# Optimization experiments

Measured on AMD Instinct MI355X. Metric: run time of the kernel, lower is better.

The kernel has to match this reference:

```python
import jax, jax.numpy as jnp
import numpy as np

D_MODEL = 1024
BS, K = 16, 64


def setup_inputs() -> dict:
    key = jax.random.key(0)
    k1, k2 = jax.random.split(key)
    Mp_cls = jax.random.normal(k1, (BS, K, D_MODEL), dtype=jnp.float32)
    mask_p = jnp.ones((BS, K, 4, K), dtype=bool)  # unused (no rnk_transformer)
    # nn.Linear(4*d_model, 3, bias=False) weight: [3, 4*d_model]
    W = jax.random.normal(k2, (3, 4 * D_MODEL), dtype=jnp.float32) * (4 * D_MODEL) ** -0.5
    return {"Mp_cls": Mp_cls, "mask_p": mask_p, "W": W}


def reference(Mp_cls, mask_p, W):
    # Pairwise scores: feature at [b,i,j] = cat(A[b,j], A[b,i], |A[b,j]-A[b,i]|, A[b,i]*A[b,j])
    # scores = feature @ W.T  -> [bs,K,K,3]. We split W into its 4 d_model blocks
    # so the concatenated [bs,K,K,4d] tensor is never materialized.
    d = Mp_cls.shape[-1]
    W1, W2, W3, W4 = W[:, :d], W[:, d:2 * d], W[:, 2 * d:3 * d], W[:, 3 * d:]
    t1 = jnp.einsum('bjd,cd->bjc', Mp_cls, W1)[:, None, :, :]          # from unsqueeze(1).expand
    t2 = jnp.einsum('bid,cd->bic', Mp_cls, W2)[:, :, None, :]          # from unsqueeze(2).expand
    diff = jnp.abs(Mp_cls[:, None, :, :] - Mp_cls[:, :, None, :])      # [bs,K,K,d]
    t3 = jnp.einsum('bijd,cd->bijc', diff, W3)
    t4 = jnp.einsum('bid,bjd,cd->bijc', Mp_cls, Mp_cls, W4)            # elementwise product term
    return t1 + t2 + t3 + t4  # [bs, K, K, 3]
```

## Files before the change

kernel.cpp:

```cpp
#include <hip/hip_runtime.h>

#define D_MODEL 1024
#define KK 64
#define BSZ 16

__global__ __launch_bounds__(256) void precompute_rows(
    const float* __restrict__ Mp, const float* __restrict__ W,
    float* __restrict__ P12)
{
    const int wave = (blockIdx.x * 256 + threadIdx.x) >> 6;
    const int lane = threadIdx.x & 63;
    const float* row = Mp + (size_t)wave * D_MODEL;

    float s[6] = {0.f, 0.f, 0.f, 0.f, 0.f, 0.f};
#pragma unroll
    for (int k = 0; k < 4; ++k) {
        const int d = k * 256 + lane * 4;
        const float4 m = *reinterpret_cast<const float4*>(row + d);
#pragma unroll
        for (int c = 0; c < 3; ++c) {
            const float4 w1 = *reinterpret_cast<const float4*>(W + c * 4096 + d);
            const float4 w2 = *reinterpret_cast<const float4*>(W + c * 4096 + 1024 + d);
            s[c]     += m.x * w1.x + m.y * w1.y + m.z * w1.z + m.w * w1.w;
            s[3 + c] += m.x * w2.x + m.y * w2.y + m.z * w2.z + m.w * w2.w;
        }
    }
#pragma unroll
    for (int off = 32; off; off >>= 1)
#pragma unroll
        for (int t = 0; t < 6; ++t)
            s[t] += __shfl_xor(s[t], off, 64);

    if (lane < 3) {
        P12[wave * 3 + lane]        = s[lane];
        P12[3072 + wave * 3 + lane] = s[3 + lane];
    }
}

__global__ __launch_bounds__(256) void pair_kernel(
    const float* __restrict__ Mp, const float* __restrict__ W,
    const float* __restrict__ P12, float* __restrict__ out)
{
    const int b   = blockIdx.x >> 6;
    const int i   = blockIdx.x & 63;
    const int wid = threadIdx.x >> 6;
    const int lane = threadIdx.x & 63;

    const float* batch = Mp + (size_t)b * KK * D_MODEL;
    const float* rowi  = batch + i * D_MODEL;

    float4 mi[4], w3[3][4], w4[3][4];
#pragma unroll
    for (int k = 0; k < 4; ++k) {
        const int d = k * 256 + lane * 4;
        mi[k] = *reinterpret_cast<const float4*>(rowi + d);
#pragma unroll
        for (int c = 0; c < 3; ++c) {
            w3[c][k] = *reinterpret_cast<const float4*>(W + c * 4096 + 2048 + d);
            w4[c][k] = *reinterpret_cast<const float4*>(W + c * 4096 + 3072 + d);
        }
    }

    const float p2c0 = P12[3072 + (b * 64 + i) * 3 + 0];
    const float p2c1 = P12[3072 + (b * 64 + i) * 3 + 1];
    const float p2c2 = P12[3072 + (b * 64 + i) * 3 + 2];

#pragma unroll 1
    for (int jj = 0; jj < 16; ++jj) {
        const int j = wid * 16 + jj;
        const float* rowj = batch + j * D_MODEL;

        float s3[3] = {0.f, 0.f, 0.f};
        float s4[3] = {0.f, 0.f, 0.f};
#pragma unroll
        for (int k = 0; k < 4; ++k) {
            const float4 mj = *reinterpret_cast<const float4*>(rowj + k * 256 + lane * 4);
#define TERM(E)                                                                \
            {                                                                  \
                const float dabs = fabsf(mi[k].E - mj.E);                      \
                const float prod = mi[k].E * mj.E;                             \
                s3[0] += dabs * w3[0][k].E;                                    \
                s3[1] += dabs * w3[1][k].E;                                    \
                s3[2] += dabs * w3[2][k].E;                                    \
                s4[0] += prod * w4[0][k].E;                                    \
                s4[1] += prod * w4[1][k].E;                                    \
                s4[2] += prod * w4[2][k].E;                                    \
            }
            TERM(x) TERM(y) TERM(z) TERM(w)
#undef TERM
        }

#pragma unroll
        for (int off = 32; off; off >>= 1) {
#pragma unroll
            for (int t = 0; t < 3; ++t) {
                s3[t] += __shfl_xor(s3[t], off, 64);
                s4[t] += __shfl_xor(s4[t], off, 64);
            }
        }

        if (lane < 3) {
            const int c = lane;
            out[(((size_t)b * 64 + i) * 64 + j) * 3 + c] =
                P12[(b * 64 + j) * 3 + c] + ((c == 0) ? p2c0 : (c == 1) ? p2c1 : p2c2)
                + s3[c] + s4[c];
        }
    }
}

extern "C" void kernel_launch(void* const* d_in, const int* in_sizes, int n_in,
                              void* d_out, int out_size, void* d_ws, size_t ws_size,
                              hipStream_t stream)
{
    const float* Mp = (const float*)d_in[0];
    const float* W  = (const float*)d_in[2];
    float* out = (float*)d_out;
    float* P12 = (float*)d_ws;

    precompute_rows<<<256, 256, 0, stream>>>(Mp, W, P12);
    pair_kernel<<<BSZ * KK, 256, 0, stream>>>(Mp, W, P12, out);
}
```

Before: 101.3 us.

## Exploit pair symmetry to compute only upper-triangular i,j pairs

```diff
diff --git a/kernel.cpp b/kernel.cpp
--- a/kernel.cpp
+++ b/kernel.cpp
@@ -8,22 +8,19 @@
     const float* __restrict__ Mp, const float* __restrict__ W,
     float* __restrict__ P12)
 {
-    const int wave = (blockIdx.x * 256 + threadIdx.x) >> 6;
+    const int row  = blockIdx.x;
+    const int wid  = threadIdx.x >> 6;
     const int lane = threadIdx.x & 63;
-    const float* row = Mp + (size_t)wave * D_MODEL;
+    const int d    = wid * 256 + lane * 4;
 
-    float s[6] = {0.f, 0.f, 0.f, 0.f, 0.f, 0.f};
+    const float4 m = *reinterpret_cast<const float4*>(Mp + (size_t)row * D_MODEL + d);
+    float s[6];
 #pragma unroll
-    for (int k = 0; k < 4; ++k) {
-        const int d = k * 256 + lane * 4;
-        const float4 m = *reinterpret_cast<const float4*>(row + d);
-#pragma unroll
-        for (int c = 0; c < 3; ++c) {
-            const float4 w1 = *reinterpret_cast<const float4*>(W + c * 4096 + d);
-            const float4 w2 = *reinterpret_cast<const float4*>(W + c * 4096 + 1024 + d);
-            s[c]     += m.x * w1.x + m.y * w1.y + m.z * w1.z + m.w * w1.w;
-            s[3 + c] += m.x * w2.x + m.y * w2.y + m.z * w2.z + m.w * w2.w;
-        }
+    for (int c = 0; c < 3; ++c) {
+        const float4 w1 = *reinterpret_cast<const float4*>(W + c * 4096 + d);
+        const float4 w2 = *reinterpret_cast<const float4*>(W + c * 4096 + 1024 + d);
+        s[c]     = m.x * w1.x + m.y * w1.y + m.z * w1.z + m.w * w1.w;
+        s[3 + c] = m.x * w2.x + m.y * w2.y + m.z * w2.z + m.w * w2.w;
     }
 #pragma unroll
     for (int off = 32; off; off >>= 1)
@@ -31,60 +28,80 @@
         for (int t = 0; t < 6; ++t)
             s[t] += __shfl_xor(s[t], off, 64);
 
-    if (lane < 3) {
-        P12[wave * 3 + lane]        = s[lane];
-        P12[3072 + wave * 3 + lane] = s[3 + lane];
+    __shared__ float part[4][6];
+    if (lane == 0) {
+#pragma unroll
+        for (int t = 0; t < 6; ++t) part[wid][t] = s[t];
+    }
+    __syncthreads();
+    if (threadIdx.x < 6) {
+        const int t = threadIdx.x;
+        const float v = part[0][t] + part[1][t] + part[2][t] + part[3][t];
+        if (t < 3) P12[row * 3 + t]              = v;
+        else       P12[3072 + row * 3 + (t - 3)] = v;
     }
 }
 
-__global__ __launch_bounds__(256) void pair_kernel(
+__device__ __forceinline__ int tri_start(int i) { return (i * (129 - i)) >> 1; }
+
+__global__ __launch_bounds__(256, 2) void pair_kernel(
     const float* __restrict__ Mp, const float* __restrict__ W,
     const float* __restrict__ P12, float* __restrict__ out)
 {
-    const int b   = blockIdx.x >> 6;
-    const int i   = blockIdx.x & 63;
-    const int wid = threadIdx.x >> 6;
+    const int b    = blockIdx.x;
+    const int slot = blockIdx.y;
+    const int wid  = threadIdx.x >> 6;
     const int lane = threadIdx.x & 63;
 
     const float* batch = Mp + (size_t)b * KK * D_MODEL;
-    const float* rowi  = batch + i * D_MODEL;
+    float*       outb  = out + (size_t)b * KK * KK * 3;
+    const float* P1    = P12 + b * KK * 3;
+    const float* P2    = P12 + 3072 + b * KK * 3;
 
-    float4 mi[4], w3[3][4], w4[3][4];
+    float4 w3[3][4], w4[3][4];
 #pragma unroll
     for (int k = 0; k < 4; ++k) {
         const int d = k * 256 + lane * 4;
-        mi[k] = *reinterpret_cast<const float4*>(rowi + d);
 #pragma unroll
         for (int c = 0; c < 3; ++c) {
             w3[c][k] = *reinterpret_cast<const float4*>(W + c * 4096 + 2048 + d);
             w4[c][k] = *reinterpret_cast<const float4*>(W + c * 4096 + 3072 + d);
         }
     }
+#define KEEP4(f) asm volatile("" : "+v"(f.x), "+v"(f.y), "+v"(f.z), "+v"(f.w))
+#pragma unroll
+    for (int c = 0; c < 3; ++c)
+#pragma unroll
+        for (int k = 0; k < 4; ++k) { KEEP4(w3[c][k]); KEEP4(w4[c][k]); }
+#undef KEEP4
 
-    const float p2c0 = P12[3072 + (b * 64 + i) * 3 + 0];
-    const float p2c1 = P12[3072 + (b * 64 + i) * 3 + 1];
-    const float p2c2 = P12[3072 + (b * 64 + i) * 3 + 2];
+    const int p0 = slot * 32 + wid * 8;
+    int i = (int)((129.0f - sqrtf(16641.0f - 8.0f * (float)p0)) * 0.5f);
+    if (i > 63) i = 63;
+    if (i < 0)  i = 0;
+    while (tri_start(i + 1) <= p0) ++i;
+    while (tri_start(i) > p0) --i;
+    int j = i + (p0 - tri_start(i));
 
-#pragma unroll 1
-    for (int jj = 0; jj < 16; ++jj) {
-        const int j = wid * 16 + jj;
+    float4 mi[4];
+#pragma unroll
+    for (int k = 0; k < 4; ++k)
+        mi[k] = *reinterpret_cast<const float4*>(batch + i * D_MODEL + k * 256 + lane * 4);
+
+#pragma unroll 2
+    for (int t = 0; t < 8; ++t) {
         const float* rowj = batch + j * D_MODEL;
-
-        float s3[3] = {0.f, 0.f, 0.f};
-        float s4[3] = {0.f, 0.f, 0.f};
+        float sc0 = 0.f, sc1 = 0.f, sc2 = 0.f;
 #pragma unroll
         for (int k = 0; k < 4; ++k) {
             const float4 mj = *reinterpret_cast<const float4*>(rowj + k * 256 + lane * 4);
-#define TERM(E)                                                                \
-            {                                                                  \
-                const float dabs = fabsf(mi[k].E - mj.E);                      \
-                const float prod = mi[k].E * mj.E;                             \
-                s3[0] += dabs * w3[0][k].E;                                    \
-                s3[1] += dabs * w3[1][k].E;                                    \
-                s3[2] += dabs * w3[2][k].E;                                    \
-                s4[0] += prod * w4[0][k].E;                                    \
-                s4[1] += prod * w4[1][k].E;                                    \
-                s4[2] += prod * w4[2][k].E;                                    \
+#define TERM(E)                                                      \
+            {                                                        \
+                const float dabs = fabsf(mi[k].E - mj.E);            \
+                const float prod = mi[k].E * mj.E;                   \
+                sc0 += dabs * w3[0][k].E;  sc0 += prod * w4[0][k].E; \
+                sc1 += dabs * w3[1][k].E;  sc1 += prod * w4[1][k].E; \
+                sc2 += dabs * w3[2][k].E;  sc2 += prod * w4[2][k].E; \
             }
             TERM(x) TERM(y) TERM(z) TERM(w)
 #undef TERM
@@ -92,18 +109,27 @@
 
 #pragma unroll
         for (int off = 32; off; off >>= 1) {
-#pragma unroll
-            for (int t = 0; t < 3; ++t) {
-                s3[t] += __shfl_xor(s3[t], off, 64);
-                s4[t] += __shfl_xor(s4[t], off, 64);
-            }
+            sc0 += __shfl_xor(sc0, off, 64);
+            sc1 += __shfl_xor(sc1, off, 64);
+            sc2 += __shfl_xor(sc2, off, 64);
         }
 
         if (lane < 3) {
             const int c = lane;
-            out[(((size_t)b * 64 + i) * 64 + j) * 3 + c] =
-                P12[(b * 64 + j) * 3 + c] + ((c == 0) ? p2c0 : (c == 1) ? p2c1 : p2c2)
-                + s3[c] + s4[c];
+            const float sc = (c == 0) ? sc0 : (c == 1) ? sc1 : sc2;
+            outb[(i * KK + j) * 3 + c] = P1[j * 3 + c] + P2[i * 3 + c] + sc;
+            outb[(j * KK + i) * 3 + c] = P1[i * 3 + c] + P2[j * 3 + c] + sc;
+        }
+
+        ++j;
+        if (j == KK) {
+            ++i;
+            if (i < KK) {
+                j = i;
+#pragma unroll
+                for (int k = 0; k < 4; ++k)
+                    mi[k] = *reinterpret_cast<const float4*>(batch + i * D_MODEL + k * 256 + lane * 4);
+            }
         }
     }
 }
@@ -117,6 +143,6 @@
     float* out = (float*)d_out;
     float* P12 = (float*)d_ws;
 
-    precompute_rows<<<256, 256, 0, stream>>>(Mp, W, P12);
-    pair_kernel<<<BSZ * KK, 256, 0, stream>>>(Mp, W, P12, out);
+    precompute_rows<<<1024, 256, 0, stream>>>(Mp, W, P12);
+    pair_kernel<<<dim3(BSZ, 65), 256, 0, stream>>>(Mp, W, P12, out);
 }
```

Result: faster. 81.62 us (-19.4%).

## Transpose Mp per batch and map j to lanes to drop per-pair shuffle reductions

Applied to the files above, without the earlier changes.

```diff
diff --git a/kernel.cpp b/kernel.cpp
--- a/kernel.cpp
+++ b/kernel.cpp
@@ -4,106 +4,133 @@
 #define KK 64
 #define BSZ 16
 
-__global__ __launch_bounds__(256) void precompute_rows(
+__global__ __launch_bounds__(256) void prep_kernel(
     const float* __restrict__ Mp, const float* __restrict__ W,
-    float* __restrict__ P12)
+    float* __restrict__ MpT, float* __restrict__ P12)
 {
-    const int wave = (blockIdx.x * 256 + threadIdx.x) >> 6;
-    const int lane = threadIdx.x & 63;
-    const float* row = Mp + (size_t)wave * D_MODEL;
+    const int b = blockIdx.x;
+    const int y = blockIdx.y;
+    const int t = threadIdx.x;
 
-    float s[6] = {0.f, 0.f, 0.f, 0.f, 0.f, 0.f};
+    if (y < 16) {
+        __shared__ float tile[64 * 65];
+        const int d0 = y * 64;
+        const float* __restrict__ src = Mp + (size_t)b * (KK * D_MODEL);
 #pragma unroll
-    for (int k = 0; k < 4; ++k) {
-        const int d = k * 256 + lane * 4;
-        const float4 m = *reinterpret_cast<const float4*>(row + d);
+        for (int p = 0; p < 4; ++p) {
+            const int idx = p * 256 + t;
+            const int j   = idx >> 4;
+            const int c4  = (idx & 15) * 4;
+            const float4 v = *reinterpret_cast<const float4*>(src + j * D_MODEL + d0 + c4);
+            float* dst = &tile[j * 65 + c4];
+            dst[0] = v.x; dst[1] = v.y; dst[2] = v.z; dst[3] = v.w;
+        }
+        __syncthreads();
+        float* __restrict__ dstb = MpT + (size_t)b * (KK * D_MODEL) + (size_t)d0 * KK;
 #pragma unroll
-        for (int c = 0; c < 3; ++c) {
-            const float4 w1 = *reinterpret_cast<const float4*>(W + c * 4096 + d);
-            const float4 w2 = *reinterpret_cast<const float4*>(W + c * 4096 + 1024 + d);
-            s[c]     += m.x * w1.x + m.y * w1.y + m.z * w1.z + m.w * w1.w;
-            s[3 + c] += m.x * w2.x + m.y * w2.y + m.z * w2.z + m.w * w2.w;
+        for (int p = 0; p < 4; ++p) {
+            const int idx = p * 256 + t;
+            const int d   = idx >> 4;
+            const int j4  = (idx & 15) * 4;
+            float4 v;
+            v.x = tile[(j4 + 0) * 65 + d];
+            v.y = tile[(j4 + 1) * 65 + d];
+            v.z = tile[(j4 + 2) * 65 + d];
+            v.w = tile[(j4 + 3) * 65 + d];
+            *reinterpret_cast<float4*>(dstb + d * KK + j4) = v;
         }
-    }
+    } else {
+        __shared__ float part[64][6][4];
+        const int rl = t >> 2;
+        const int q  = t & 3;
+        const float* __restrict__ rp = Mp + ((size_t)(b * KK + rl)) * D_MODEL + q * 256;
+        float s[6] = {0.f, 0.f, 0.f, 0.f, 0.f, 0.f};
+        for (int kk = 0; kk < 64; ++kk) {
+            const float4 m = *reinterpret_cast<const float4*>(rp + kk * 4);
 #pragma unroll
-    for (int off = 32; off; off >>= 1)
+            for (int c = 0; c < 3; ++c) {
+                const float4 w1 = *reinterpret_cast<const float4*>(W + c * 4096 + q * 256 + kk * 4);
+                const float4 w2 = *reinterpret_cast<const float4*>(W + c * 4096 + 1024 + q * 256 + kk * 4);
+                s[c]     += m.x * w1.x + m.y * w1.y + m.z * w1.z + m.w * w1.w;
+                s[3 + c] += m.x * w2.x + m.y * w2.y + m.z * w2.z + m.w * w2.w;
+            }
+        }
 #pragma unroll
-        for (int t = 0; t < 6; ++t)
-            s[t] += __shfl_xor(s[t], off, 64);
-
-    if (lane < 3) {
-        P12[wave * 3 + lane]        = s[lane];
-        P12[3072 + wave * 3 + lane] = s[3 + lane];
+        for (int u = 0; u < 6; ++u) part[rl][u][q] = s[u];
+        __syncthreads();
+        if (t < 128) {
+            const int rr   = t >> 1;
+            const int half = t & 1;
+#pragma unroll
+            for (int c = 0; c < 3; ++c) {
+                const float v = part[rr][half * 3 + c][0] + part[rr][half * 3 + c][1]
+                              + part[rr][half * 3 + c][2] + part[rr][half * 3 + c][3];
+                P12[(half ? 3072 : 0) + (b * KK + rr) * 3 + c] = v;
+            }
+        }
     }
 }
 
 __global__ __launch_bounds__(256) void pair_kernel(
     const float* __restrict__ Mp, const float* __restrict__ W,
-    const float* __restrict__ P12, float* __restrict__ out)
+    const float* __restrict__ MpT, const float* __restrict__ P12,
+    float* __restrict__ out)
 {
-    const int b   = blockIdx.x >> 6;
-    const int i   = blockIdx.x & 63;
-    const int wid = threadIdx.x >> 6;
+    __shared__ float red[4][2][3][64];
+
+    const int b    = blockIdx.x;
+    const int i0   = blockIdx.y * 2;
     const int lane = threadIdx.x & 63;
+    const int wid  = threadIdx.x >> 6;
+    const int uwid = __builtin_amdgcn_readfirstlane(wid);
 
-    const float* batch = Mp + (size_t)b * KK * D_MODEL;
-    const float* rowi  = batch + i * D_MODEL;
+    const int dbase = uwid * 256;
+    const float* __restrict__ mjp  = MpT + (size_t)b * (KK * D_MODEL) + (size_t)dbase * KK + lane;
+    const float* __restrict__ mi0p = Mp + ((size_t)(b * KK + i0)) * D_MODEL + dbase;
+    const float* __restrict__ mi1p = mi0p + D_MODEL;
+    const float* __restrict__ w3b  = W + 2048 + dbase;
+    const float* __restrict__ w4b  = W + 3072 + dbase;
 
-    float4 mi[4], w3[3][4], w4[3][4];
-#pragma unroll
-    for (int k = 0; k < 4; ++k) {
-        const int d = k * 256 + lane * 4;
-        mi[k] = *reinterpret_cast<const float4*>(rowi + d);
+    float a00 = 0.f, a01 = 0.f, a02 = 0.f;
+    float a10 = 0.f, a11 = 0.f, a12 = 0.f;
+
+#pragma unroll 8
+    for (int k = 0; k < 256; ++k) {
+        const float mj  = mjp[k * KK];
+        const float mi0 = mi0p[k];
+        const float mi1 = mi1p[k];
+        const float u0 = w3b[k], u1 = w3b[4096 + k], u2 = w3b[8192 + k];
+        const float v0 = w4b[k], v1 = w4b[4096 + k], v2 = w4b[8192 + k];
+
+        const float d0 = mi0 - mj;
+        const float p0 = mi0 * mj;
+        a00 = fmaf(fabsf(d0), u0, a00);  a00 = fmaf(p0, v0, a00);
+        a01 = fmaf(fabsf(d0), u1, a01);  a01 = fmaf(p0, v1, a01);
+        a02 = fmaf(fabsf(d0), u2, a02);  a02 = fmaf(p0, v2, a02);
+
+        const float d1 = mi1 - mj;
+        const float p1 = mi1 * mj;
+        a10 = fmaf(fabsf(d1), u0, a10);  a10 = fmaf(p1, v0, a10);
+        a11 = fmaf(fabsf(d1), u1, a11);  a11 = fmaf(p1, v1, a11);
+        a12 = fmaf(fabsf(d1), u2, a12);  a12 = fmaf(p1, v2, a12);
+    }
+
+    red[wid][0][0][lane] = a00;  red[wid][0][1][lane] = a01;  red[wid][0][2][lane] = a02;
+    red[wid][1][0][lane] = a10;  red[wid][1][1][lane] = a11;  red[wid][1][2][lane] = a12;
+    __syncthreads();
+
+    if (wid < 2) {
+        const int i = i0 + wid;
+        const float p2c0 = P12[3072 + (b * KK + i) * 3 + 0];
+        const float p2c1 = P12[3072 + (b * KK + i) * 3 + 1];
+        const float p2c2 = P12[3072 + (b * KK + i) * 3 + 2];
+        float* __restrict__ orow = out + (((size_t)(b * KK + i)) * KK + lane) * 3;
 #pragma unroll
         for (int c = 0; c < 3; ++c) {
-            w3[c][k] = *reinterpret_cast<const float4*>(W + c * 4096 + 2048 + d);
-            w4[c][k] = *reinterpret_cast<const float4*>(W + c * 4096 + 3072 + d);
-        }
-    }
-
-    const float p2c0 = P12[3072 + (b * 64 + i) * 3 + 0];
-    const float p2c1 = P12[3072 + (b * 64 + i) * 3 + 1];
-    const float p2c2 = P12[3072 + (b * 64 + i) * 3 + 2];
-
-#pragma unroll 1
-    for (int jj = 0; jj < 16; ++jj) {
-        const int j = wid * 16 + jj;
-        const float* rowj = batch + j * D_MODEL;
-
-        float s3[3] = {0.f, 0.f, 0.f};
-        float s4[3] = {0.f, 0.f, 0.f};
-#pragma unroll
-        for (int k = 0; k < 4; ++k) {
-            const float4 mj = *reinterpret_cast<const float4*>(rowj + k * 256 + lane * 4);
-#define TERM(E)                                                                \
-            {                                                                  \
-                const float dabs = fabsf(mi[k].E - mj.E);                      \
-                const float prod = mi[k].E * mj.E;                             \
-                s3[0] += dabs * w3[0][k].E;                                    \
-                s3[1] += dabs * w3[1][k].E;                                    \
-                s3[2] += dabs * w3[2][k].E;                                    \
-                s4[0] += prod * w4[0][k].E;                                    \
-                s4[1] += prod * w4[1][k].E;                                    \
-                s4[2] += prod * w4[2][k].E;                                    \
-            }
-            TERM(x) TERM(y) TERM(z) TERM(w)
-#undef TERM
-        }
-
-#pragma unroll
-        for (int off = 32; off; off >>= 1) {
-#pragma unroll
-            for (int t = 0; t < 3; ++t) {
-                s3[t] += __shfl_xor(s3[t], off, 64);
-                s4[t] += __shfl_xor(s4[t], off, 64);
-            }
-        }
-
-        if (lane < 3) {
-            const int c = lane;
-            out[(((size_t)b * 64 + i) * 64 + j) * 3 + c] =
-                P12[(b * 64 + j) * 3 + c] + ((c == 0) ? p2c0 : (c == 1) ? p2c1 : p2c2)
-                + s3[c] + s4[c];
+            const float s = red[0][wid][c][lane] + red[1][wid][c][lane]
+                          + red[2][wid][c][lane] + red[3][wid][c][lane];
+            const float p2 = (c == 0) ? p2c0 : (c == 1) ? p2c1 : p2c2;
+            orow[c] = s + P12[(b * KK + lane) * 3 + c] + p2;
         }
     }
 }
@@ -115,8 +142,10 @@
     const float* Mp = (const float*)d_in[0];
     const float* W  = (const float*)d_in[2];
     float* out = (float*)d_out;
-    float* P12 = (float*)d_ws;
 
-    precompute_rows<<<256, 256, 0, stream>>>(Mp, W, P12);
-    pair_kernel<<<BSZ * KK, 256, 0, stream>>>(Mp, W, P12, out);
+    float* MpT = (float*)d_ws;
+    float* P12 = MpT + (size_t)BSZ * KK * D_MODEL;
+
+    prep_kernel<<<dim3(BSZ, 17), 256, 0, stream>>>(Mp, W, MpT, P12);
+    pair_kernel<<<dim3(BSZ, 32), 256, 0, stream>>>(Mp, W, MpT, P12, out);
 }
```

Result: slower. 142.4 us (+40.5%).
